# Kernel tuning notes

Measured on AMD Instinct MI355X. Metric: run time of the kernel, lower is better.

## Reference

```python
import jax, jax.numpy as jnp
import numpy as np
from jax import lax

RADIUS = 0.2
NSAMPLE = 32


def ball_query(radius, nsample, xyz, new_xyz):
    """Vectorized equivalent of the torch nested-loop ball_query.
    xyz: (B,N,3), new_xyz: (B,M,3) -> idx (B,M,nsample) int32.
    Semantics: first `nsample` in-radius indices in ascending order;
    if fewer than nsample, pad with the first valid index; if none, zeros.
    """
    N = xyz.shape[1]
    # squared distances (B,M,N) via ||a||^2 + ||b||^2 - 2 a.b
    dist_sq = (jnp.sum(new_xyz * new_xyz, axis=-1)[:, :, None]
               + jnp.sum(xyz * xyz, axis=-1)[:, None, :]
               - 2.0 * jnp.einsum('bmd,bnd->bmn', new_xyz, xyz))
    mask = dist_sq < (radius * radius)
    # score = point index if in ball else sentinel N; smallest nsample scores
    scores = jnp.where(mask, jnp.arange(N, dtype=jnp.int32), jnp.int32(N))
    neg_vals, _ = lax.top_k(-scores, nsample)   # ascending valid indices first
    cand = -neg_vals                            # (B,M,nsample)
    first = cand[..., :1]                       # first (smallest) valid index or N
    valid = cand < N
    fill = jnp.where(first < N, first, 0)       # pad value (0 if no neighbor)
    return jnp.where(valid, cand, fill)


def group(features, idx):
    # features (B,C,N), idx (B,M,ns) -> (B,C,M,ns)
    return jax.vmap(lambda f, i: f[:, i])(features, idx)


def setup_inputs() -> dict:
    key = jax.random.key(0)
    k1, k2, k3 = jax.random.split(key, 3)
    xyz = jax.random.uniform(k1, (8, 8192, 3), dtype=jnp.float32)
    new_xyz = jax.random.uniform(k2, (8, 2048, 3), dtype=jnp.float32)
    features = jax.random.normal(k3, (8, 128, 8192), dtype=jnp.float32)
    return {"xyz": xyz, "new_xyz": new_xyz, "features": features}


def reference(xyz, new_xyz, features):
    idx = ball_query(RADIUS, NSAMPLE, xyz, new_xyz)          # (B,M,ns)
    xyz_t = jnp.transpose(xyz, (0, 2, 1))                    # (B,3,N)
    grouped_xyz = group(xyz_t, idx)                          # (B,3,M,ns)
    grouped_xyz = grouped_xyz - jnp.transpose(new_xyz, (0, 2, 1))[..., None]
    grouped_features = group(features, idx)                  # (B,C,M,ns)
    # use_xyz=True -> concat along channel dim
    return jnp.concatenate([grouped_xyz, grouped_features], axis=1)
```

## Files before the change

### kernel.cpp

```cpp
#include <hip/hip_runtime.h>

#define B_      8
#define N_      8192
#define M_      2048
#define S_      32
#define C_FEAT  128
#define C_OUT   131
#define G_      8

__device__ float g_ft[(size_t)B_ * N_ * C_FEAT];
__device__ float4 g_selc[(size_t)B_ * M_ * S_];

typedef float f32x4_t __attribute__((ext_vector_type(4)));
__device__ __forceinline__ void store_nt(float* p, float4 v) {
    f32x4_t x; x.x = v.x; x.y = v.y; x.z = v.z; x.w = v.w;
    __builtin_nontemporal_store(x, (f32x4_t*)p);
}

__global__ __launch_bounds__(256) void transpose_kernel(
    const float* __restrict__ f)
{
    __shared__ float tile[64][68];
    int t = threadIdx.x;
    int n0 = blockIdx.x * 64, c0 = blockIdx.y * 64, b = blockIdx.z;

    int nt = t & 15, cr0 = t >> 4;
    #pragma unroll
    for (int pass = 0; pass < 4; ++pass) {
        int cr = cr0 + pass * 16;
        float4 v = *((const float4*)&f[((size_t)(b * C_FEAT + c0 + cr)) * N_ + n0 + nt * 4]);
        *((float4*)&tile[cr][nt * 4]) = v;
    }
    __syncthreads();
    int ct = t & 15, nr0 = t >> 4;
    #pragma unroll
    for (int pass = 0; pass < 4; ++pass) {
        int nr = nr0 + pass * 16;
        float4 v;
        v.x = tile[ct*4+0][nr];
        v.y = tile[ct*4+1][nr];
        v.z = tile[ct*4+2][nr];
        v.w = tile[ct*4+3][nr];
        *((float4*)&g_ft[((size_t)(b * N_ + n0 + nr)) * C_FEAT + c0 + ct * 4]) = v;
    }
}

__global__ __launch_bounds__(256) void ballq_kernel(
    const float* __restrict__ xyz,
    const float* __restrict__ new_xyz)
{
    __shared__ unsigned long long s_mask[8];
    __shared__ int s_fin[32];
    __shared__ float s_cx[32], s_cy[32], s_cz[32];

    unsigned i = blockIdx.x;
    unsigned b = i & 7u, m = i >> 3;
    unsigned w = threadIdx.x >> 6, lane = threadIdx.x & 63u;

    const float* q = new_xyz + (b * M_ + m) * 3;
    float qx = q[0], qy = q[1], qz = q[2];
    float qq = __fadd_rn(__fadd_rn(__fmul_rn(qx,qx), __fmul_rn(qy,qy)), __fmul_rn(qz,qz));

    const float* P = xyz + (size_t)b * N_ * 3;

    int done = 0;
    for (int base = 0; base < N_ && done < S_; base += 512) {
        int n0 = base + (int)(w * 64u + lane);
        int n1 = n0 + 256;
        float px0 = P[n0*3+0], py0 = P[n0*3+1], pz0 = P[n0*3+2];
        float px1 = P[n1*3+0], py1 = P[n1*3+1], pz1 = P[n1*3+2];

        float pp0 = __fadd_rn(__fadd_rn(__fmul_rn(px0,px0), __fmul_rn(py0,py0)), __fmul_rn(pz0,pz0));
        float dt0 = __fadd_rn(__fadd_rn(__fmul_rn(qz,pz0), __fmul_rn(qy,py0)), __fmul_rn(qx,px0));
        float d0  = __fsub_rn(__fadd_rn(qq, pp0), __fmul_rn(2.0f, dt0));
        float pp1 = __fadd_rn(__fadd_rn(__fmul_rn(px1,px1), __fmul_rn(py1,py1)), __fmul_rn(pz1,pz1));
        float dt1 = __fadd_rn(__fadd_rn(__fmul_rn(qz,pz1), __fmul_rn(qy,py1)), __fmul_rn(qx,px1));
        float d1  = __fsub_rn(__fadd_rn(qq, pp1), __fmul_rn(2.0f, dt1));

        unsigned long long mk0 = __ballot(d0 < 0.04f);
        unsigned long long mk1 = __ballot(d1 < 0.04f);
        if (lane == 0) { s_mask[w] = mk0; s_mask[4 + w] = mk1; }
        __syncthreads();

        int c[8], tot = 0;
        #pragma unroll
        for (int k = 0; k < 8; k++) { c[k] = __popcll(s_mask[k]); tot += c[k]; }
        int pre0 = done, pre1 = done;
        #pragma unroll
        for (int k = 0; k < 8; k++) {
            if (k < (int)w)     pre0 += c[k];
            if (k < (int)(4+w)) pre1 += c[k];
        }
        if ((mk0 >> lane) & 1ull) {
            int slot = pre0 + __popcll(mk0 & ((1ull << lane) - 1ull));
            if (slot < S_) { s_fin[slot] = n0; s_cx[slot] = px0; s_cy[slot] = py0; s_cz[slot] = pz0; }
        }
        if ((mk1 >> lane) & 1ull) {
            int slot = pre1 + __popcll(mk1 & ((1ull << lane) - 1ull));
            if (slot < S_) { s_fin[slot] = n1; s_cx[slot] = px1; s_cy[slot] = py1; s_cz[slot] = pz1; }
        }
        done += tot;
        __syncthreads();
    }

    int total = (done < S_) ? done : S_;
    if ((int)threadIdx.x >= total && threadIdx.x < S_) {
        if (done > 0) {
            s_fin[threadIdx.x] = s_fin[0];
            s_cx[threadIdx.x] = s_cx[0]; s_cy[threadIdx.x] = s_cy[0]; s_cz[threadIdx.x] = s_cz[0];
        } else {
            s_fin[threadIdx.x] = 0;
            s_cx[threadIdx.x] = P[0]; s_cy[threadIdx.x] = P[1]; s_cz[threadIdx.x] = P[2];
        }
    }
    __syncthreads();

    if (threadIdx.x < S_) {
        int s = (int)threadIdx.x;
        float4 v;
        v.x = s_cx[s]; v.y = s_cy[s]; v.z = s_cz[s];
        v.w = __int_as_float(s_fin[s]);
        g_selc[((size_t)(b * M_ + m)) * S_ + s] = v;
    }
}

__global__ __launch_bounds__(512, 4) void group_kernel(
    const float* __restrict__ new_xyz,
    float* __restrict__ out)
{
    __shared__ float s_cx[G_][33], s_cy[G_][33], s_cz[G_][33];
    __shared__ int   s_fin[G_][33];
    __shared__ float sT[32][256];

    unsigned i = blockIdx.x;
    unsigned b = i & 7u;
    unsigned m0 = (i >> 3) * G_;
    unsigned t = threadIdx.x;

    if (t < 256) {
        float4 v = g_selc[((size_t)(b * M_ + m0)) * S_ + t];
        unsigned qi = t >> 5, s = t & 31u;
        s_cx[qi][s] = v.x; s_cy[qi][s] = v.y; s_cz[qi][s] = v.z;
        s_fin[qi][s] = __float_as_int(v.w);
    }
    __syncthreads();

    if (t < 192) {
        unsigned ch = t >> 6, l = t & 63u, qi = l >> 3, s4 = (l & 7u) * 4u;
        float qc = new_xyz[((size_t)(b * M_ + m0 + qi)) * 3 + ch];
        const float* sc = (ch == 0) ? s_cx[qi] : (ch == 1) ? s_cy[qi] : s_cz[qi];
        float4 v;
        v.x = __fsub_rn(sc[s4 + 0], qc);
        v.y = __fsub_rn(sc[s4 + 1], qc);
        v.z = __fsub_rn(sc[s4 + 2], qc);
        v.w = __fsub_rn(sc[s4 + 3], qc);
        size_t off = (((size_t)(b * C_OUT + ch)) * M_ + (m0 + qi)) * S_ + s4;
        store_nt(out + off, v);
    }

    unsigned p = t >> 1, h = t & 1u;
    unsigned qg = p >> 5, sg = p & 31u;
    const float* grow = g_ft + ((size_t)(b * N_ + s_fin[qg][sg])) * C_FEAT + h * 16u;

    for (int k = 0; k < 4; ++k) {
        const float4* src = (const float4*)(grow + k * 32);
        float4 v0 = src[0], v1 = src[1], v2 = src[2], v3 = src[3];
        unsigned cb = h * 16u;
        sT[cb +  0][p] = v0.x; sT[cb +  1][p] = v0.y; sT[cb +  2][p] = v0.z; sT[cb +  3][p] = v0.w;
        sT[cb +  4][p] = v1.x; sT[cb +  5][p] = v1.y; sT[cb +  6][p] = v1.z; sT[cb +  7][p] = v1.w;
        sT[cb +  8][p] = v2.x; sT[cb +  9][p] = v2.y; sT[cb + 10][p] = v2.z; sT[cb + 11][p] = v2.w;
        sT[cb + 12][p] = v3.x; sT[cb + 13][p] = v3.y; sT[cb + 14][p] = v3.z; sT[cb + 15][p] = v3.w;
        __syncthreads();
        #pragma unroll
        for (int rep = 0; rep < 4; ++rep) {
            unsigned idx = rep * 512u + t;
            unsigned chl = idx >> 6;
            unsigned l4  = (idx & 63u) * 4u;
            float4 v = *((const float4*)&sT[chl][l4]);
            size_t off = (((size_t)(b * C_OUT + 3 + k * 32 + chl)) * M_ + m0) * S_ + l4;
            store_nt(out + off, v);
        }
        __syncthreads();
    }
}

extern "C" void kernel_launch(void* const* d_in, const int* in_sizes, int n_in,
                              void* d_out, int out_size, void* d_ws, size_t ws_size,
                              hipStream_t stream) {
    const float* xyz      = (const float*)d_in[0];
    const float* new_xyz  = (const float*)d_in[1];
    const float* features = (const float*)d_in[2];
    float* out = (float*)d_out;

    transpose_kernel<<<dim3(N_ / 64, C_FEAT / 64, B_), dim3(256), 0, stream>>>(features);
    ballq_kernel<<<dim3(B_ * M_), dim3(256), 0, stream>>>(xyz, new_xyz);
    group_kernel<<<dim3(B_ * M_ / G_), dim3(512), 0, stream>>>(new_xyz, out);
}
```

Before: 351.9 us.

## Fuse ball query into group kernel with one wave per query

Merges the ball-query and grouping kernels into one. Each 64-lane wavefront now scans points for its own query, using ballot prefix counts and no block-wide barriers, and writes the selected indices and coordinates straight to shared memory. This removes the g_selc global round trip and one kernel launch. Feature-row loads are also software-pipelined one chunk ahead. The cost is that waves within a block can finish their scans at different times, and more registers are live.

```diff
diff --git a/kernel.cpp b/kernel.cpp
--- a/kernel.cpp
+++ b/kernel.cpp
@@ -9,7 +9,6 @@
 #define G_      8
 
 __device__ float g_ft[(size_t)B_ * N_ * C_FEAT];
-__device__ float4 g_selc[(size_t)B_ * M_ * S_];
 
 typedef float f32x4_t __attribute__((ext_vector_type(4)));
 __device__ __forceinline__ void store_nt(float* p, float4 v) {
@@ -45,131 +44,105 @@
     }
 }
 
-__global__ __launch_bounds__(256) void ballq_kernel(
+__global__ __launch_bounds__(512, 4) void fused_kernel(
     const float* __restrict__ xyz,
-    const float* __restrict__ new_xyz)
-{
-    __shared__ unsigned long long s_mask[8];
-    __shared__ int s_fin[32];
-    __shared__ float s_cx[32], s_cy[32], s_cz[32];
-
-    unsigned i = blockIdx.x;
-    unsigned b = i & 7u, m = i >> 3;
-    unsigned w = threadIdx.x >> 6, lane = threadIdx.x & 63u;
-
-    const float* q = new_xyz + (b * M_ + m) * 3;
-    float qx = q[0], qy = q[1], qz = q[2];
-    float qq = __fadd_rn(__fadd_rn(__fmul_rn(qx,qx), __fmul_rn(qy,qy)), __fmul_rn(qz,qz));
-
-    const float* P = xyz + (size_t)b * N_ * 3;
-
-    int done = 0;
-    for (int base = 0; base < N_ && done < S_; base += 512) {
-        int n0 = base + (int)(w * 64u + lane);
-        int n1 = n0 + 256;
-        float px0 = P[n0*3+0], py0 = P[n0*3+1], pz0 = P[n0*3+2];
-        float px1 = P[n1*3+0], py1 = P[n1*3+1], pz1 = P[n1*3+2];
-
-        float pp0 = __fadd_rn(__fadd_rn(__fmul_rn(px0,px0), __fmul_rn(py0,py0)), __fmul_rn(pz0,pz0));
-        float dt0 = __fadd_rn(__fadd_rn(__fmul_rn(qz,pz0), __fmul_rn(qy,py0)), __fmul_rn(qx,px0));
-        float d0  = __fsub_rn(__fadd_rn(qq, pp0), __fmul_rn(2.0f, dt0));
-        float pp1 = __fadd_rn(__fadd_rn(__fmul_rn(px1,px1), __fmul_rn(py1,py1)), __fmul_rn(pz1,pz1));
-        float dt1 = __fadd_rn(__fadd_rn(__fmul_rn(qz,pz1), __fmul_rn(qy,py1)), __fmul_rn(qx,px1));
-        float d1  = __fsub_rn(__fadd_rn(qq, pp1), __fmul_rn(2.0f, dt1));
-
-        unsigned long long mk0 = __ballot(d0 < 0.04f);
-        unsigned long long mk1 = __ballot(d1 < 0.04f);
-        if (lane == 0) { s_mask[w] = mk0; s_mask[4 + w] = mk1; }
-        __syncthreads();
-
-        int c[8], tot = 0;
-        #pragma unroll
-        for (int k = 0; k < 8; k++) { c[k] = __popcll(s_mask[k]); tot += c[k]; }
-        int pre0 = done, pre1 = done;
-        #pragma unroll
-        for (int k = 0; k < 8; k++) {
-            if (k < (int)w)     pre0 += c[k];
-            if (k < (int)(4+w)) pre1 += c[k];
-        }
-        if ((mk0 >> lane) & 1ull) {
-            int slot = pre0 + __popcll(mk0 & ((1ull << lane) - 1ull));
-            if (slot < S_) { s_fin[slot] = n0; s_cx[slot] = px0; s_cy[slot] = py0; s_cz[slot] = pz0; }
-        }
-        if ((mk1 >> lane) & 1ull) {
-            int slot = pre1 + __popcll(mk1 & ((1ull << lane) - 1ull));
-            if (slot < S_) { s_fin[slot] = n1; s_cx[slot] = px1; s_cy[slot] = py1; s_cz[slot] = pz1; }
-        }
-        done += tot;
-        __syncthreads();
-    }
-
-    int total = (done < S_) ? done : S_;
-    if ((int)threadIdx.x >= total && threadIdx.x < S_) {
-        if (done > 0) {
-            s_fin[threadIdx.x] = s_fin[0];
-            s_cx[threadIdx.x] = s_cx[0]; s_cy[threadIdx.x] = s_cy[0]; s_cz[threadIdx.x] = s_cz[0];
-        } else {
-            s_fin[threadIdx.x] = 0;
-            s_cx[threadIdx.x] = P[0]; s_cy[threadIdx.x] = P[1]; s_cz[threadIdx.x] = P[2];
-        }
-    }
-    __syncthreads();
-
-    if (threadIdx.x < S_) {
-        int s = (int)threadIdx.x;
-        float4 v;
-        v.x = s_cx[s]; v.y = s_cy[s]; v.z = s_cz[s];
-        v.w = __int_as_float(s_fin[s]);
-        g_selc[((size_t)(b * M_ + m)) * S_ + s] = v;
-    }
-}
-
-__global__ __launch_bounds__(512, 4) void group_kernel(
     const float* __restrict__ new_xyz,
     float* __restrict__ out)
 {
-    __shared__ float s_cx[G_][33], s_cy[G_][33], s_cz[G_][33];
-    __shared__ int   s_fin[G_][33];
-    __shared__ float sT[32][256];
+    __shared__ float4 s_sel[G_][S_];
+    __shared__ float  s_q[G_][3];
+    __shared__ int    s_done[G_];
+    __shared__ float  sT[32][256];
 
     unsigned i = blockIdx.x;
     unsigned b = i & 7u;
     unsigned m0 = (i >> 3) * G_;
     unsigned t = threadIdx.x;
+    unsigned w = t >> 6, lane = t & 63u;
+
+    const float* q = new_xyz + ((size_t)(b * M_ + m0 + w)) * 3;
+    float qx = q[0], qy = q[1], qz = q[2];
+    if (lane == 0) { s_q[w][0] = qx; s_q[w][1] = qy; s_q[w][2] = qz; }
+    float qq = __fadd_rn(__fadd_rn(__fmul_rn(qx,qx), __fmul_rn(qy,qy)), __fmul_rn(qz,qz));
+    const float* P = xyz + (size_t)b * N_ * 3;
+
+    int done = 0;
+    for (int nb = 0; nb < N_ && done < S_; nb += 256) {
+        float px[4], py[4], pz[4];
+        #pragma unroll
+        for (int r = 0; r < 4; ++r) {
+            int n = nb + r * 64 + (int)lane;
+            px[r] = P[n*3+0]; py[r] = P[n*3+1]; pz[r] = P[n*3+2];
+        }
+        #pragma unroll
+        for (int r = 0; r < 4; ++r) {
+            float pp = __fadd_rn(__fadd_rn(__fmul_rn(px[r],px[r]), __fmul_rn(py[r],py[r])), __fmul_rn(pz[r],pz[r]));
+            float dt = __fadd_rn(__fadd_rn(__fmul_rn(qz,pz[r]), __fmul_rn(qy,py[r])), __fmul_rn(qx,px[r]));
+            float d  = __fsub_rn(__fadd_rn(qq, pp), __fmul_rn(2.0f, dt));
+            unsigned long long mk = __ballot(d < 0.04f);
+            if ((mk >> lane) & 1ull) {
+                int slot = done + __popcll(mk & ((1ull << lane) - 1ull));
+                if (slot < S_) {
+                    float4 v;
+                    v.x = px[r]; v.y = py[r]; v.z = pz[r];
+                    v.w = __int_as_float(nb + r * 64 + (int)lane);
+                    s_sel[w][slot] = v;
+                }
+            }
+            done += (int)__popcll(mk);
+        }
+    }
+    if (lane == 0) s_done[w] = done;
+    __syncthreads();
 
     if (t < 256) {
-        float4 v = g_selc[((size_t)(b * M_ + m0)) * S_ + t];
-        unsigned qi = t >> 5, s = t & 31u;
-        s_cx[qi][s] = v.x; s_cy[qi][s] = v.y; s_cz[qi][s] = v.z;
-        s_fin[qi][s] = __float_as_int(v.w);
+        int w2 = (int)(t >> 5), s = (int)(t & 31u);
+        int dn = s_done[w2];
+        int total = dn < S_ ? dn : S_;
+        if (s >= total) {
+            float4 v;
+            if (dn > 0) v = s_sel[w2][0];
+            else { v.x = P[0]; v.y = P[1]; v.z = P[2]; v.w = __int_as_float(0); }
+            s_sel[w2][s] = v;
+        }
     }
     __syncthreads();
 
     if (t < 192) {
         unsigned ch = t >> 6, l = t & 63u, qi = l >> 3, s4 = (l & 7u) * 4u;
-        float qc = new_xyz[((size_t)(b * M_ + m0 + qi)) * 3 + ch];
-        const float* sc = (ch == 0) ? s_cx[qi] : (ch == 1) ? s_cy[qi] : s_cz[qi];
+        float qc = s_q[qi][ch];
+        const float* sp = (const float*)&s_sel[qi][0];
         float4 v;
-        v.x = __fsub_rn(sc[s4 + 0], qc);
-        v.y = __fsub_rn(sc[s4 + 1], qc);
-        v.z = __fsub_rn(sc[s4 + 2], qc);
-        v.w = __fsub_rn(sc[s4 + 3], qc);
+        v.x = __fsub_rn(sp[(s4 + 0) * 4 + ch], qc);
+        v.y = __fsub_rn(sp[(s4 + 1) * 4 + ch], qc);
+        v.z = __fsub_rn(sp[(s4 + 2) * 4 + ch], qc);
+        v.w = __fsub_rn(sp[(s4 + 3) * 4 + ch], qc);
         size_t off = (((size_t)(b * C_OUT + ch)) * M_ + (m0 + qi)) * S_ + s4;
         store_nt(out + off, v);
     }
 
     unsigned p = t >> 1, h = t & 1u;
     unsigned qg = p >> 5, sg = p & 31u;
-    const float* grow = g_ft + ((size_t)(b * N_ + s_fin[qg][sg])) * C_FEAT + h * 16u;
+    float4 selv = s_sel[qg][sg];
+    int n = __float_as_int(selv.w);
+    const float* grow = g_ft + ((size_t)(b * N_ + n)) * C_FEAT + h * 16u;
+
+    float4 r0 = ((const float4*)grow)[0];
+    float4 r1 = ((const float4*)grow)[1];
+    float4 r2 = ((const float4*)grow)[2];
+    float4 r3 = ((const float4*)grow)[3];
 
     for (int k = 0; k < 4; ++k) {
-        const float4* src = (const float4*)(grow + k * 32);
-        float4 v0 = src[0], v1 = src[1], v2 = src[2], v3 = src[3];
+        float4 n0, n1, n2, n3;
+        if (k < 3) {
+            const float4* src = (const float4*)(grow + (k + 1) * 32);
+            n0 = src[0]; n1 = src[1]; n2 = src[2]; n3 = src[3];
+        }
         unsigned cb = h * 16u;
-        sT[cb +  0][p] = v0.x; sT[cb +  1][p] = v0.y; sT[cb +  2][p] = v0.z; sT[cb +  3][p] = v0.w;
-        sT[cb +  4][p] = v1.x; sT[cb +  5][p] = v1.y; sT[cb +  6][p] = v1.z; sT[cb +  7][p] = v1.w;
-        sT[cb +  8][p] = v2.x; sT[cb +  9][p] = v2.y; sT[cb + 10][p] = v2.z; sT[cb + 11][p] = v2.w;
-        sT[cb + 12][p] = v3.x; sT[cb + 13][p] = v3.y; sT[cb + 14][p] = v3.z; sT[cb + 15][p] = v3.w;
+        sT[cb +  0][p] = r0.x; sT[cb +  1][p] = r0.y; sT[cb +  2][p] = r0.z; sT[cb +  3][p] = r0.w;
+        sT[cb +  4][p] = r1.x; sT[cb +  5][p] = r1.y; sT[cb +  6][p] = r1.z; sT[cb +  7][p] = r1.w;
+        sT[cb +  8][p] = r2.x; sT[cb +  9][p] = r2.y; sT[cb + 10][p] = r2.z; sT[cb + 11][p] = r2.w;
+        sT[cb + 12][p] = r3.x; sT[cb + 13][p] = r3.y; sT[cb + 14][p] = r3.z; sT[cb + 15][p] = r3.w;
         __syncthreads();
         #pragma unroll
         for (int rep = 0; rep < 4; ++rep) {
@@ -181,6 +154,7 @@
             store_nt(out + off, v);
         }
         __syncthreads();
+        r0 = n0; r1 = n1; r2 = n2; r3 = n3;
     }
 }
 
@@ -193,6 +167,5 @@
     float* out = (float*)d_out;
 
     transpose_kernel<<<dim3(N_ / 64, C_FEAT / 64, B_), dim3(256), 0, stream>>>(features);
-    ballq_kernel<<<dim3(B_ * M_), dim3(256), 0, stream>>>(xyz, new_xyz);
-    group_kernel<<<dim3(B_ * M_ / G_), dim3(512), 0, stream>>>(new_xyz, out);
+    fused_kernel<<<dim3(B_ * M_ / G_), dim3(512), 0, stream>>>(xyz, new_xyz, out);
 }
```

After: 324.2 us. -7.9%, faster.
